# Performance work log

Measured on AMD Instinct MI355X. Metric: run time of the kernel, lower is better.

The kernel has to match this reference:

```python
import jax, jax.numpy as jnp
import numpy as np

B, N, IN_F, OUT_F, REL_DIM, NUM_REL = 4, 2048, 256, 128, 10, 6
D = OUT_F // 2  # internal_dim
ALPHA = 0.2
LAMBDA_INIT = 0.8 - 0.6 * float(np.exp(-0.3 * 1))  # depth=1
EPS = 1e-5


def setup_inputs() -> dict:
    key = jax.random.key(0)
    ks = jax.random.split(key, 16)
    return {
        "h": jax.random.normal(ks[0], (B, N, IN_F), jnp.float32),
        "adj": jax.random.randint(ks[1], (B, N, N), 0, NUM_REL, jnp.int32),
        "W": jax.random.normal(ks[2], (IN_F, OUT_F), jnp.float32) * (1.414 / np.sqrt(IN_F)),
        "a_left_pos": jax.random.normal(ks[3], (D,), jnp.float32) * 0.1,
        "a_right_pos": jax.random.normal(ks[4], (D,), jnp.float32) * 0.1,
        "a_left_neg": jax.random.normal(ks[5], (D,), jnp.float32) * 0.1,
        "a_right_neg": jax.random.normal(ks[6], (D,), jnp.float32) * 0.1,
        "rel_emb": jax.random.normal(ks[7], (NUM_REL, REL_DIM), jnp.float32),
        "a_rel_pos": jax.random.normal(ks[8], (REL_DIM,), jnp.float32) * 0.3,
        "a_rel_neg": jax.random.normal(ks[9], (REL_DIM,), jnp.float32) * 0.3,
        "lambda_left1": jax.random.normal(ks[10], (D,), jnp.float32) * 0.1,
        "lambda_right1": jax.random.normal(ks[11], (D,), jnp.float32) * 0.1,
        "lambda_left2": jax.random.normal(ks[12], (D,), jnp.float32) * 0.1,
        "lambda_right2": jax.random.normal(ks[13], (D,), jnp.float32) * 0.1,
        "ln_gamma": jnp.ones((OUT_F,), jnp.float32),
        "ln_beta": jnp.zeros((OUT_F,), jnp.float32),
    }


def _leaky_relu(x):
    return jnp.where(x >= 0, x, ALPHA * x)


def reference(h, adj, W, a_left_pos, a_right_pos, a_left_neg, a_right_neg,
              rel_emb, a_rel_pos, a_rel_neg,
              lambda_left1, lambda_right1, lambda_left2, lambda_right2,
              ln_gamma, ln_beta):
    Wh = jnp.einsum('bnf,fo->bno', h, W)              # [B,N,OUT_F]
    Wh4 = Wh.reshape(B, N, 2, D)
    Wh_pos, Wh_neg = Wh4[:, :, 0, :], Wh4[:, :, 1, :]  # [B,N,D]

    # e[b,i,j] = left[b,i] + right[b,j] + rel_score[adj[b,i,j]]
    # relation Linear(rel_dim,1) applied to embedding rows == per-relation scalar lookup
    rel_score_pos = rel_emb @ a_rel_pos               # [NUM_REL]
    rel_score_neg = rel_emb @ a_rel_neg
    e_pos = (Wh_pos @ a_left_pos)[:, :, None] + (Wh_pos @ a_right_pos)[:, None, :] + rel_score_pos[adj]
    e_neg = (Wh_neg @ a_left_neg)[:, :, None] + (Wh_neg @ a_right_neg)[:, None, :] + rel_score_neg[adj]

    neg_inf = jnp.float32(-9e15)
    mask = adj > 0
    attn_pos = jax.nn.softmax(jnp.where(mask, _leaky_relu(e_pos), neg_inf), axis=2)
    attn_neg = jax.nn.softmax(jnp.where(mask, _leaky_relu(e_neg), neg_inf), axis=2)

    lam1 = jnp.exp(jnp.sum(lambda_left1 * lambda_right1))
    lam2 = jnp.exp(jnp.sum(lambda_left2 * lambda_right2))
    lambda_full = lam1 - lam2 + LAMBDA_INIT
    attention = attn_pos - lambda_full * attn_neg     # [B,N,N]

    Wh_v = jnp.concatenate([Wh_pos, Wh_neg], axis=-1)  # [B,N,OUT_F]
    h_prime = jnp.einsum('bij,bjo->bio', attention, Wh_v)

    mu = jnp.mean(h_prime, axis=-1, keepdims=True)
    var = jnp.mean(jnp.square(h_prime - mu), axis=-1, keepdims=True)
    h_prime = (h_prime - mu) * jax.lax.rsqrt(var + EPS) * ln_gamma + ln_beta
    h_prime = h_prime * (1.0 - LAMBDA_INIT)
    return jax.nn.gelu(h_prime, approximate=False), attention
```

## Files before the change

### kernel.cpp

```cpp
#include <hip/hip_runtime.h>
#include <math.h>

typedef short bf16x8 __attribute__((ext_vector_type(8)));
typedef float f32x4  __attribute__((ext_vector_type(4)));

constexpr int   B_    = 4;
constexpr int   N_    = 2048;
constexpr int   INF_  = 256;
constexpr int   OUTF_ = 128;
constexpr float LAMBDA_INIT_ = 0.35550906759096926f;
constexpr float OUT_SCALE_   = 0.64449093240903074f;
constexpr float EPS_         = 1e-5f;
constexpr float LOG2E_       = 1.44269504088896340736f;

__device__ inline unsigned short f2bf(float x) {
  unsigned u = __float_as_uint(x);
  u += 0x7fffu + ((u >> 16) & 1u);
  return (unsigned short)(u >> 16);
}
__device__ inline unsigned pack2(float a, float b) {
  return (unsigned)f2bf(a) | ((unsigned)f2bf(b) << 16);
}

__global__ void scalars_kernel(const float* __restrict__ rel_emb,
                               const float* __restrict__ a_rel_pos,
                               const float* __restrict__ a_rel_neg,
                               const float* __restrict__ ll1, const float* __restrict__ lr1,
                               const float* __restrict__ ll2, const float* __restrict__ lr2,
                               float* __restrict__ scal) {
  int lane = threadIdx.x;
  float p1 = ll1[lane] * lr1[lane];
  float p2 = ll2[lane] * lr2[lane];
  #pragma unroll
  for (int off = 32; off; off >>= 1) { p1 += __shfl_xor(p1, off); p2 += __shfl_xor(p2, off); }
  if (lane == 0) scal[12] = expf(p1) - expf(p2) + LAMBDA_INIT_;
  if (lane < 6) {
    float sp = 0.f, sn = 0.f;
    for (int k = 0; k < 10; ++k) {
      float rv = rel_emb[lane * 10 + k];
      sp += rv * a_rel_pos[k];
      sn += rv * a_rel_neg[k];
    }
    scal[lane]     = sp * LOG2E_;
    scal[6 + lane] = sn * LOG2E_;
  }
}

__global__ __launch_bounds__(256) void wh_dots_kernel(
    const float* __restrict__ h, const float* __restrict__ W,
    const float* __restrict__ alp, const float* __restrict__ arp,
    const float* __restrict__ aln, const float* __restrict__ arn,
    float* __restrict__ Wh, unsigned short* __restrict__ WhvT,
    float* __restrict__ lposv, float* __restrict__ rposv,
    float* __restrict__ lnegv, float* __restrict__ rnegv) {
  __shared__ __align__(16) float hT[INF_][20];
  const int t = threadIdx.x;
  const size_t row0 = (size_t)blockIdx.x * 16;
  #pragma unroll
  for (int i = 0; i < 16; ++i) hT[t][i] = h[(row0 + i) * INF_ + t];
  __syncthreads();
  const int c  = t & 127;
  const int rg = t >> 7;
  float acc[8] = {0.f, 0.f, 0.f, 0.f, 0.f, 0.f, 0.f, 0.f};
  #pragma unroll 4
  for (int k = 0; k < INF_; ++k) {
    float wv = W[k * OUTF_ + c];
    const float4* hp = reinterpret_cast<const float4*>(&hT[k][rg * 8]);
    float4 h0 = hp[0], h1 = hp[1];
    acc[0] += h0.x * wv; acc[1] += h0.y * wv; acc[2] += h0.z * wv; acc[3] += h0.w * wv;
    acc[4] += h1.x * wv; acc[5] += h1.y * wv; acc[6] += h1.z * wv; acc[7] += h1.w * wv;
  }
  #pragma unroll
  for (int r = 0; r < 8; ++r) Wh[(row0 + rg * 8 + r) * OUTF_ + c] = acc[r];
  uint4 pk;
  pk.x = pack2(acc[0], acc[1]); pk.y = pack2(acc[2], acc[3]);
  pk.z = pack2(acc[4], acc[5]); pk.w = pack2(acc[6], acc[7]);
  const int b  = (int)(row0 >> 11);
  const int n0 = (int)(row0 & 2047) + rg * 8;
  *reinterpret_cast<uint4*>(WhvT + ((size_t)b * OUTF_ + c) * N_ + n0) = pk;

  const int lane = t & 63;
  const int wv   = t >> 6;
  const bool pos = (wv & 1) == 0;
  const float al = pos ? alp[lane] : aln[lane];
  const float ar = pos ? arp[lane] : arn[lane];
  float sl[8], sr2[8];
  #pragma unroll
  for (int r = 0; r < 8; ++r) { sl[r] = acc[r] * al; sr2[r] = acc[r] * ar; }
  #pragma unroll
  for (int off = 32; off; off >>= 1) {
    #pragma unroll
    for (int r = 0; r < 8; ++r) {
      sl[r]  += __shfl_xor(sl[r],  off);
      sr2[r] += __shfl_xor(sr2[r], off);
    }
  }
  if (lane == 0) {
    #pragma unroll
    for (int r = 0; r < 8; ++r) {
      const int node = (int)row0 + rg * 8 + r;
      if (pos) { lposv[node] = sl[r] * LOG2E_; rposv[node] = sr2[r] * LOG2E_; }
      else     { lnegv[node] = sl[r] * LOG2E_; rnegv[node] = sr2[r] * LOG2E_; }
    }
  }
}

__global__ __launch_bounds__(512) void attn_v3d(
    const int* __restrict__ adj,
    const float* __restrict__ lposv, const float* __restrict__ rposv,
    const float* __restrict__ lnegv, const float* __restrict__ rnegv,
    const float* __restrict__ scal, float* __restrict__ out1) {
  __shared__ float sums[16];
  const int t = threadIdx.x;
  const int lane = t & 63;
  const int wv = t >> 6;
  const int flat = blockIdx.x;
  const int b = flat >> 11;

  const float lam = scal[12];
  float srcP = -1.0e30f, srcN = -1.0e30f;
  if (lane >= 1 && lane <= 5) { srcP = scal[lane]; srcN = scal[6 + lane]; }
  const int iSrcP = __float_as_int(srcP);
  const int iSrcN = __float_as_int(srcN);

  const float lP = lposv[flat];
  const float lN = lnegv[flat];
  const int j0 = t * 4;
  int4   av4 = *reinterpret_cast<const int4*>(adj + (size_t)flat * N_ + j0);
  float4 rp4 = *reinterpret_cast<const float4*>(rposv + b * N_ + j0);
  float4 rn4 = *reinterpret_cast<const float4*>(rnegv + b * N_ + j0);
  int   av[4] = {av4.x, av4.y, av4.z, av4.w};
  float rp[4] = {rp4.x, rp4.y, rp4.z, rp4.w};
  float rn[4] = {rn4.x, rn4.y, rn4.z, rn4.w};

  float p[4], n[4];
  #pragma unroll
  for (int q = 0; q < 4; ++q) {
    float rsp = __int_as_float(__builtin_amdgcn_ds_bpermute(av[q] << 2, iSrcP));
    float rsn = __int_as_float(__builtin_amdgcn_ds_bpermute(av[q] << 2, iSrcN));
    float e  = lP + rp[q] + rsp;
    float en = lN + rn[q] + rsn;
    e  = fmaxf(e, 0.2f * e);
    en = fmaxf(en, 0.2f * en);
    p[q] = __builtin_amdgcn_exp2f(e);
    n[q] = __builtin_amdgcn_exp2f(en);
  }
  float sP = (p[0] + p[1]) + (p[2] + p[3]);
  float sN = (n[0] + n[1]) + (n[2] + n[3]);
  #pragma unroll
  for (int off = 32; off; off >>= 1) { sP += __shfl_xor(sP, off); sN += __shfl_xor(sN, off); }
  if (lane == 0) { sums[wv] = sP; sums[8 + wv] = sN; }
  __syncthreads();
  float vP = sums[lane & 7];
  vP += __shfl_xor(vP, 1); vP += __shfl_xor(vP, 2); vP += __shfl_xor(vP, 4);
  float vN = sums[8 + (lane & 7)];
  vN += __shfl_xor(vN, 1); vN += __shfl_xor(vN, 2); vN += __shfl_xor(vN, 4);
  const float s1 = 1.f / vP;
  const float s2 = -lam / vN;

  float a[4];
  #pragma unroll
  for (int q = 0; q < 4; ++q) a[q] = p[q] * s1 + n[q] * s2;
  float* o1 = out1 + (size_t)flat * N_ + j0;
  *reinterpret_cast<float4*>(o1) = make_float4(a[0], a[1], a[2], a[3]);
}

__global__ __launch_bounds__(512) void pv_v5b(
    const float* __restrict__ attn, const unsigned short* __restrict__ WhvT,
    const float* __restrict__ gamma, const float* __restrict__ beta,
    float* __restrict__ out0) {
  __shared__ __align__(16) uint4 A4[2][16 * 32];
  __shared__ __align__(16) float hp[16][132];
  const int t = threadIdx.x;
  const int lane = t & 63;
  const int w = t >> 6;
  const int bi = blockIdx.x;
  const int b  = bi >> 7;
  const int i0 = (bi & 127) * 16;

  const int sr = t >> 5;
  const int sj = t & 31;
  const float4* src4 = reinterpret_cast<const float4*>(
      attn + ((size_t)(b * N_ + i0 + sr)) * N_ + sj * 8);
  const int swz = sr & 7;
  const int ui = sr * 32 + (sj ^ swz);

  const int bl  = lane & 15;
  const int kg  = lane >> 4;
  const int ch  = w * 16 + bl;
  const unsigned short* Bp = WhvT + ((size_t)b * OUTF_ + ch) * N_ + kg * 8;
  f32x4 acc0 = {0.f, 0.f, 0.f, 0.f};
  f32x4 acc1 = {0.f, 0.f, 0.f, 0.f};
  const int arow = bl * 32;
  const int aswz = bl & 7;

  {
    float4 s0 = src4[0], s1 = src4[1];
    uint4 u;
    u.x = pack2(s0.x, s0.y); u.y = pack2(s0.z, s0.w);
    u.z = pack2(s1.x, s1.y); u.w = pack2(s1.z, s1.w);
    A4[0][ui] = u;
  }
  __syncthreads();

  for (int c = 0; c < 8; ++c) {
    const int cur = c & 1;
    float4 s0, s1;
    if (c < 7) {
      const int o = (c + 1) * 64;
      s0 = src4[o]; s1 = src4[o + 1];
    }
    const unsigned short* bp = Bp + c * 256;
    #pragma unroll
    for (int kk = 0; kk < 8; ++kk) {
      bf16x8 a  = *reinterpret_cast<const bf16x8*>(&A4[cur][arow + ((kk * 4 + kg) ^ aswz)]);
      bf16x8 bv = *reinterpret_cast<const bf16x8*>(bp + kk * 32);
      if (cur == 0) acc0 = __builtin_amdgcn_mfma_f32_16x16x32_bf16(a, bv, acc0, 0, 0, 0);
      else          acc1 = __builtin_amdgcn_mfma_f32_16x16x32_bf16(a, bv, acc1, 0, 0, 0);
    }
    if (c < 7) {
      uint4 u;
      u.x = pack2(s0.x, s0.y); u.y = pack2(s0.z, s0.w);
      u.z = pack2(s1.x, s1.y); u.w = pack2(s1.z, s1.w);
      A4[cur ^ 1][ui] = u;
    }
    __syncthreads();
  }

  #pragma unroll
  for (int q = 0; q < 4; ++q) hp[kg * 4 + q][ch] = acc0[q] + acc1[q];
  __syncthreads();

  const int row = t >> 5;
  const int c0  = t & 31;
  float v[4], s = 0.f, sq = 0.f;
  #pragma unroll
  for (int e = 0; e < 4; ++e) {
    v[e] = hp[row][c0 + e * 32];
    s += v[e]; sq += v[e] * v[e];
  }
  #pragma unroll
  for (int off = 16; off; off >>= 1) { s += __shfl_xor(s, off); sq += __shfl_xor(sq, off); }
  const float mu  = s  * (1.f / 128.f);
  const float var = sq * (1.f / 128.f) - mu * mu;
  const float inv = rsqrtf(var + EPS_);
  float* orow = out0 + ((size_t)(b * N_ + i0 + row)) * OUTF_;
  #pragma unroll
  for (int e = 0; e < 4; ++e) {
    const int chh = c0 + e * 32;
    float y = (v[e] - mu) * inv * gamma[chh] + beta[chh];
    y *= OUT_SCALE_;
    orow[chh] = 0.5f * y * (1.f + erff(y * 0.70710678118654752f));
  }
}

extern "C" void kernel_launch(void* const* d_in, const int* in_sizes, int n_in,
                              void* d_out, int out_size, void* d_ws, size_t ws_size,
                              hipStream_t stream) {
  (void)in_sizes; (void)n_in; (void)out_size; (void)ws_size;
  const float* h        = (const float*)d_in[0];
  const int*   adj      = (const int*)d_in[1];
  const float* W        = (const float*)d_in[2];
  const float* alp      = (const float*)d_in[3];
  const float* arp      = (const float*)d_in[4];
  const float* aln      = (const float*)d_in[5];
  const float* arn      = (const float*)d_in[6];
  const float* rel_emb  = (const float*)d_in[7];
  const float* a_rel_p  = (const float*)d_in[8];
  const float* a_rel_n  = (const float*)d_in[9];
  const float* ll1      = (const float*)d_in[10];
  const float* lr1      = (const float*)d_in[11];
  const float* ll2      = (const float*)d_in[12];
  const float* lr2      = (const float*)d_in[13];
  const float* gamma    = (const float*)d_in[14];
  const float* beta     = (const float*)d_in[15];

  float* out0 = (float*)d_out;
  float* out1 = out0 + (size_t)B_ * N_ * OUTF_;

  float* ws    = (float*)d_ws;
  float* scal  = ws;
  float* lposv = ws + 32;
  float* rposv = lposv + B_ * N_;
  float* lnegv = rposv + B_ * N_;
  float* rnegv = lnegv + B_ * N_;
  float* Wh    = rnegv + B_ * N_;
  unsigned short* WhvT = (unsigned short*)(Wh + (size_t)B_ * N_ * OUTF_);

  scalars_kernel<<<1, 64, 0, stream>>>(rel_emb, a_rel_p, a_rel_n, ll1, lr1, ll2, lr2, scal);
  wh_dots_kernel<<<(B_ * N_) / 16, 256, 0, stream>>>(h, W, alp, arp, aln, arn,
                                                     Wh, WhvT, lposv, rposv, lnegv, rnegv);
  attn_v3d<<<B_ * N_, 512, 0, stream>>>(adj, lposv, rposv, lnegv, rnegv, scal, out1);
  pv_v5b<<<B_ * (N_ / 16), 512, 0, stream>>>(out1, WhvT, gamma, beta, out0);
}
```

Baseline: 91.30 us.

## Split PV matmul along K into two partial blocks, add separate LayerNorm-GELU kernel

The attention-times-values kernel now splits the 2048-long reduction into two halves handled by separate blocks, doubling the grid from 512 to 1024 blocks. Partial sums go to a workspace buffer, and a new kernel adds the two partials and applies LayerNorm and GELU. The unused fp32 Wh store in the projection kernel is also removed. The aim is better CU occupancy on the PV stage, at the cost of an extra launch and a round trip of partial results through global memory.

```diff
diff --git a/kernel.cpp b/kernel.cpp
--- a/kernel.cpp
+++ b/kernel.cpp
@@ -50,7 +50,7 @@
     const float* __restrict__ h, const float* __restrict__ W,
     const float* __restrict__ alp, const float* __restrict__ arp,
     const float* __restrict__ aln, const float* __restrict__ arn,
-    float* __restrict__ Wh, unsigned short* __restrict__ WhvT,
+    unsigned short* __restrict__ WhvT,
     float* __restrict__ lposv, float* __restrict__ rposv,
     float* __restrict__ lnegv, float* __restrict__ rnegv) {
   __shared__ __align__(16) float hT[INF_][20];
@@ -70,8 +70,6 @@
     acc[0] += h0.x * wv; acc[1] += h0.y * wv; acc[2] += h0.z * wv; acc[3] += h0.w * wv;
     acc[4] += h1.x * wv; acc[5] += h1.y * wv; acc[6] += h1.z * wv; acc[7] += h1.w * wv;
   }
-  #pragma unroll
-  for (int r = 0; r < 8; ++r) Wh[(row0 + rg * 8 + r) * OUTF_ + c] = acc[r];
   uint4 pk;
   pk.x = pack2(acc[0], acc[1]); pk.y = pack2(acc[2], acc[3]);
   pk.z = pack2(acc[4], acc[5]); pk.w = pack2(acc[6], acc[7]);
@@ -165,30 +163,30 @@
   *reinterpret_cast<float4*>(o1) = make_float4(a[0], a[1], a[2], a[3]);
 }
 
-__global__ __launch_bounds__(512) void pv_v5b(
+__global__ __launch_bounds__(512) void pv_v7(
     const float* __restrict__ attn, const unsigned short* __restrict__ WhvT,
-    const float* __restrict__ gamma, const float* __restrict__ beta,
-    float* __restrict__ out0) {
+    float* __restrict__ hpart) {
   __shared__ __align__(16) uint4 A4[2][16 * 32];
-  __shared__ __align__(16) float hp[16][132];
   const int t = threadIdx.x;
   const int lane = t & 63;
   const int w = t >> 6;
   const int bi = blockIdx.x;
-  const int b  = bi >> 7;
-  const int i0 = (bi & 127) * 16;
+  const int tile = bi >> 1;
+  const int kb   = bi & 1;
+  const int b  = tile >> 7;
+  const int i0 = (tile & 127) * 16;
 
   const int sr = t >> 5;
   const int sj = t & 31;
   const float4* src4 = reinterpret_cast<const float4*>(
-      attn + ((size_t)(b * N_ + i0 + sr)) * N_ + sj * 8);
+      attn + ((size_t)(b * N_ + i0 + sr)) * N_ + kb * 1024 + sj * 8);
   const int swz = sr & 7;
   const int ui = sr * 32 + (sj ^ swz);
 
   const int bl  = lane & 15;
   const int kg  = lane >> 4;
   const int ch  = w * 16 + bl;
-  const unsigned short* Bp = WhvT + ((size_t)b * OUTF_ + ch) * N_ + kg * 8;
+  const unsigned short* Bp = WhvT + ((size_t)b * OUTF_ + ch) * N_ + kb * 1024 + kg * 8;
   f32x4 acc0 = {0.f, 0.f, 0.f, 0.f};
   f32x4 acc1 = {0.f, 0.f, 0.f, 0.f};
   const int arow = bl * 32;
@@ -203,10 +201,10 @@
   }
   __syncthreads();
 
-  for (int c = 0; c < 8; ++c) {
+  for (int c = 0; c < 4; ++c) {
     const int cur = c & 1;
     float4 s0, s1;
-    if (c < 7) {
+    if (c < 3) {
       const int o = (c + 1) * 64;
       s0 = src4[o]; s1 = src4[o + 1];
     }
@@ -218,7 +216,7 @@
       if (cur == 0) acc0 = __builtin_amdgcn_mfma_f32_16x16x32_bf16(a, bv, acc0, 0, 0, 0);
       else          acc1 = __builtin_amdgcn_mfma_f32_16x16x32_bf16(a, bv, acc1, 0, 0, 0);
     }
-    if (c < 7) {
+    if (c < 3) {
       uint4 u;
       u.x = pack2(s0.x, s0.y); u.y = pack2(s0.z, s0.w);
       u.z = pack2(s1.x, s1.y); u.w = pack2(s1.z, s1.w);
@@ -227,30 +225,47 @@
     __syncthreads();
   }
 
-  #pragma unroll
-  for (int q = 0; q < 4; ++q) hp[kg * 4 + q][ch] = acc0[q] + acc1[q];
-  __syncthreads();
-
-  const int row = t >> 5;
-  const int c0  = t & 31;
-  float v[4], s = 0.f, sq = 0.f;
-  #pragma unroll
-  for (int e = 0; e < 4; ++e) {
-    v[e] = hp[row][c0 + e * 32];
+  float* hp = hpart + ((size_t)kb * B_ * N_ + (size_t)(b * N_ + i0)) * OUTF_;
+  #pragma unroll
+  for (int q = 0; q < 4; ++q) hp[(size_t)(kg * 4 + q) * OUTF_ + ch] = acc0[q] + acc1[q];
+}
+
+__global__ __launch_bounds__(256) void ln_gelu_kernel(
+    const float* __restrict__ hpart,
+    const float* __restrict__ gamma, const float* __restrict__ beta,
+    float* __restrict__ out0) {
+  const int t = threadIdx.x;
+  const int bi = blockIdx.x;
+  const int b  = bi >> 7;
+  const int i0 = (bi & 127) * 16;
+  const int row = t >> 4;
+  const int c0  = t & 15;
+
+  const size_t idx0 = ((size_t)(b * N_ + i0 + row)) * OUTF_;
+  const float* h0 = hpart + idx0;
+  const float* h1 = hpart + (size_t)B_ * N_ * OUTF_ + idx0;
+
+  float v[8], g8[8], bt8[8];
+  float s = 0.f, sq = 0.f;
+  #pragma unroll
+  for (int e = 0; e < 8; ++e) {
+    const int ch = c0 + e * 16;
+    v[e]  = h0[ch] + h1[ch];
+    g8[e] = gamma[ch];
+    bt8[e] = beta[ch];
     s += v[e]; sq += v[e] * v[e];
   }
   #pragma unroll
-  for (int off = 16; off; off >>= 1) { s += __shfl_xor(s, off); sq += __shfl_xor(sq, off); }
+  for (int off = 8; off; off >>= 1) { s += __shfl_xor(s, off); sq += __shfl_xor(sq, off); }
   const float mu  = s  * (1.f / 128.f);
   const float var = sq * (1.f / 128.f) - mu * mu;
   const float inv = rsqrtf(var + EPS_);
-  float* orow = out0 + ((size_t)(b * N_ + i0 + row)) * OUTF_;
-  #pragma unroll
-  for (int e = 0; e < 4; ++e) {
-    const int chh = c0 + e * 32;
-    float y = (v[e] - mu) * inv * gamma[chh] + beta[chh];
+  float* orow = out0 + idx0;
+  #pragma unroll
+  for (int e = 0; e < 8; ++e) {
+    float y = (v[e] - mu) * inv * g8[e] + bt8[e];
     y *= OUT_SCALE_;
-    orow[chh] = 0.5f * y * (1.f + erff(y * 0.70710678118654752f));
+    orow[c0 + e * 16] = 0.5f * y * (1.f + erff(y * 0.70710678118654752f));
   }
 }
 
@@ -284,12 +299,13 @@
   float* rposv = lposv + B_ * N_;
   float* lnegv = rposv + B_ * N_;
   float* rnegv = lnegv + B_ * N_;
-  float* Wh    = rnegv + B_ * N_;
-  unsigned short* WhvT = (unsigned short*)(Wh + (size_t)B_ * N_ * OUTF_);
+  unsigned short* WhvT = (unsigned short*)(rnegv + B_ * N_);
+  float* hpart = (float*)(WhvT + (size_t)B_ * N_ * OUTF_);
 
   scalars_kernel<<<1, 64, 0, stream>>>(rel_emb, a_rel_p, a_rel_n, ll1, lr1, ll2, lr2, scal);
   wh_dots_kernel<<<(B_ * N_) / 16, 256, 0, stream>>>(h, W, alp, arp, aln, arn,
-                                                     Wh, WhvT, lposv, rposv, lnegv, rnegv);
+                                                     WhvT, lposv, rposv, lnegv, rnegv);
   attn_v3d<<<B_ * N_, 512, 0, stream>>>(adj, lposv, rposv, lnegv, rnegv, scal, out1);
-  pv_v5b<<<B_ * (N_ / 16), 512, 0, stream>>>(out1, WhvT, gamma, beta, out0);
-}
+  pv_v7<<<B_ * (N_ / 16) * 2, 512, 0, stream>>>(out1, WhvT, hpart);
+  ln_gelu_kernel<<<B_ * (N_ / 16), 256, 0, stream>>>(hpart, gamma, beta, out0);
+}
```

Result: slower. 96.30 us (+5.5%).

## Process eight attention rows per block with adj prefetch; drop unused fp32 Wh store

Applied to the files above, without the earlier changes.

The attention kernel now handles eight rows per block instead of one. It reuses the rposv/rnegv loads across those rows and prefetches the next row's adj slice while the current row is computed. A double-buffered shared sums array keeps the per-row block reductions safe with one barrier each. The wh_dots kernel no longer writes the fp32 Wh buffer, which nothing read, saving 4 MB of stores. The cost is fewer blocks, which may reduce parallelism in a kernel that is bound by memory bandwidth.

```diff
diff --git a/kernel.cpp b/kernel.cpp
--- a/kernel.cpp
+++ b/kernel.cpp
@@ -50,7 +50,7 @@
     const float* __restrict__ h, const float* __restrict__ W,
     const float* __restrict__ alp, const float* __restrict__ arp,
     const float* __restrict__ aln, const float* __restrict__ arn,
-    float* __restrict__ Wh, unsigned short* __restrict__ WhvT,
+    unsigned short* __restrict__ WhvT,
     float* __restrict__ lposv, float* __restrict__ rposv,
     float* __restrict__ lnegv, float* __restrict__ rnegv) {
   __shared__ __align__(16) float hT[INF_][20];
@@ -70,8 +70,6 @@
     acc[0] += h0.x * wv; acc[1] += h0.y * wv; acc[2] += h0.z * wv; acc[3] += h0.w * wv;
     acc[4] += h1.x * wv; acc[5] += h1.y * wv; acc[6] += h1.z * wv; acc[7] += h1.w * wv;
   }
-  #pragma unroll
-  for (int r = 0; r < 8; ++r) Wh[(row0 + rg * 8 + r) * OUTF_ + c] = acc[r];
   uint4 pk;
   pk.x = pack2(acc[0], acc[1]); pk.y = pack2(acc[2], acc[3]);
   pk.z = pack2(acc[4], acc[5]); pk.w = pack2(acc[6], acc[7]);
@@ -105,17 +103,17 @@
   }
 }
 
-__global__ __launch_bounds__(512) void attn_v3d(
+__global__ __launch_bounds__(512) void attn_v4(
     const int* __restrict__ adj,
     const float* __restrict__ lposv, const float* __restrict__ rposv,
     const float* __restrict__ lnegv, const float* __restrict__ rnegv,
     const float* __restrict__ scal, float* __restrict__ out1) {
-  __shared__ float sums[16];
+  __shared__ float sums[2][16];
   const int t = threadIdx.x;
   const int lane = t & 63;
   const int wv = t >> 6;
-  const int flat = blockIdx.x;
-  const int b = flat >> 11;
+  const int flat0 = blockIdx.x * 8;
+  const int b = flat0 >> 11;
 
   const float lam = scal[12];
   float srcP = -1.0e30f, srcN = -1.0e30f;
@@ -123,46 +121,56 @@
   const int iSrcP = __float_as_int(srcP);
   const int iSrcN = __float_as_int(srcN);
 
-  const float lP = lposv[flat];
-  const float lN = lnegv[flat];
   const int j0 = t * 4;
-  int4   av4 = *reinterpret_cast<const int4*>(adj + (size_t)flat * N_ + j0);
   float4 rp4 = *reinterpret_cast<const float4*>(rposv + b * N_ + j0);
   float4 rn4 = *reinterpret_cast<const float4*>(rnegv + b * N_ + j0);
-  int   av[4] = {av4.x, av4.y, av4.z, av4.w};
-  float rp[4] = {rp4.x, rp4.y, rp4.z, rp4.w};
-  float rn[4] = {rn4.x, rn4.y, rn4.z, rn4.w};
-
-  float p[4], n[4];
-  #pragma unroll
-  for (int q = 0; q < 4; ++q) {
-    float rsp = __int_as_float(__builtin_amdgcn_ds_bpermute(av[q] << 2, iSrcP));
-    float rsn = __int_as_float(__builtin_amdgcn_ds_bpermute(av[q] << 2, iSrcN));
-    float e  = lP + rp[q] + rsp;
-    float en = lN + rn[q] + rsn;
-    e  = fmaxf(e, 0.2f * e);
-    en = fmaxf(en, 0.2f * en);
-    p[q] = __builtin_amdgcn_exp2f(e);
-    n[q] = __builtin_amdgcn_exp2f(en);
-  }
-  float sP = (p[0] + p[1]) + (p[2] + p[3]);
-  float sN = (n[0] + n[1]) + (n[2] + n[3]);
-  #pragma unroll
-  for (int off = 32; off; off >>= 1) { sP += __shfl_xor(sP, off); sN += __shfl_xor(sN, off); }
-  if (lane == 0) { sums[wv] = sP; sums[8 + wv] = sN; }
-  __syncthreads();
-  float vP = sums[lane & 7];
-  vP += __shfl_xor(vP, 1); vP += __shfl_xor(vP, 2); vP += __shfl_xor(vP, 4);
-  float vN = sums[8 + (lane & 7)];
-  vN += __shfl_xor(vN, 1); vN += __shfl_xor(vN, 2); vN += __shfl_xor(vN, 4);
-  const float s1 = 1.f / vP;
-  const float s2 = -lam / vN;
-
-  float a[4];
-  #pragma unroll
-  for (int q = 0; q < 4; ++q) a[q] = p[q] * s1 + n[q] * s2;
-  float* o1 = out1 + (size_t)flat * N_ + j0;
-  *reinterpret_cast<float4*>(o1) = make_float4(a[0], a[1], a[2], a[3]);
+  const float rp[4] = {rp4.x, rp4.y, rp4.z, rp4.w};
+  const float rn[4] = {rn4.x, rn4.y, rn4.z, rn4.w};
+
+  int4 avN = *reinterpret_cast<const int4*>(adj + (size_t)flat0 * N_ + j0);
+
+  #pragma unroll
+  for (int r = 0; r < 8; ++r) {
+    const int flat = flat0 + r;
+    const int4 av4 = avN;
+    if (r < 7)
+      avN = *reinterpret_cast<const int4*>(adj + (size_t)(flat + 1) * N_ + j0);
+    const float lP = lposv[flat];
+    const float lN = lnegv[flat];
+    int av[4] = {av4.x, av4.y, av4.z, av4.w};
+
+    float p[4], n[4];
+    #pragma unroll
+    for (int q = 0; q < 4; ++q) {
+      float rsp = __int_as_float(__builtin_amdgcn_ds_bpermute(av[q] << 2, iSrcP));
+      float rsn = __int_as_float(__builtin_amdgcn_ds_bpermute(av[q] << 2, iSrcN));
+      float e  = lP + rp[q] + rsp;
+      float en = lN + rn[q] + rsn;
+      e  = fmaxf(e, 0.2f * e);
+      en = fmaxf(en, 0.2f * en);
+      p[q] = __builtin_amdgcn_exp2f(e);
+      n[q] = __builtin_amdgcn_exp2f(en);
+    }
+    float sP = (p[0] + p[1]) + (p[2] + p[3]);
+    float sN = (n[0] + n[1]) + (n[2] + n[3]);
+    #pragma unroll
+    for (int off = 32; off; off >>= 1) { sP += __shfl_xor(sP, off); sN += __shfl_xor(sN, off); }
+    const int bf = r & 1;
+    if (lane == 0) { sums[bf][wv] = sP; sums[bf][8 + wv] = sN; }
+    __syncthreads();
+    float vP = sums[bf][lane & 7];
+    vP += __shfl_xor(vP, 1); vP += __shfl_xor(vP, 2); vP += __shfl_xor(vP, 4);
+    float vN = sums[bf][8 + (lane & 7)];
+    vN += __shfl_xor(vN, 1); vN += __shfl_xor(vN, 2); vN += __shfl_xor(vN, 4);
+    const float s1 = 1.f / vP;
+    const float s2 = -lam / vN;
+
+    float a[4];
+    #pragma unroll
+    for (int q = 0; q < 4; ++q) a[q] = p[q] * s1 + n[q] * s2;
+    float* o1 = out1 + (size_t)flat * N_ + j0;
+    *reinterpret_cast<float4*>(o1) = make_float4(a[0], a[1], a[2], a[3]);
+  }
 }
 
 __global__ __launch_bounds__(512) void pv_v5b(
@@ -284,12 +292,11 @@
   float* rposv = lposv + B_ * N_;
   float* lnegv = rposv + B_ * N_;
   float* rnegv = lnegv + B_ * N_;
-  float* Wh    = rnegv + B_ * N_;
-  unsigned short* WhvT = (unsigned short*)(Wh + (size_t)B_ * N_ * OUTF_);
+  unsigned short* WhvT = (unsigned short*)(rnegv + B_ * N_);
 
   scalars_kernel<<<1, 64, 0, stream>>>(rel_emb, a_rel_p, a_rel_n, ll1, lr1, ll2, lr2, scal);
   wh_dots_kernel<<<(B_ * N_) / 16, 256, 0, stream>>>(h, W, alp, arp, aln, arn,
-                                                     Wh, WhvT, lposv, rposv, lnegv, rnegv);
-  attn_v3d<<<B_ * N_, 512, 0, stream>>>(adj, lposv, rposv, lnegv, rnegv, scal, out1);
+                                                     WhvT, lposv, rposv, lnegv, rnegv);
+  attn_v4<<<(B_ * N_) / 8, 512, 0, stream>>>(adj, lposv, rposv, lnegv, rnegv, scal, out1);
   pv_v5b<<<B_ * (N_ / 16), 512, 0, stream>>>(out1, WhvT, gamma, beta, out0);
 }
```

New measurement: 91.31 us. Within noise of the previous version (+0.0%).
